# Optimization experiments

Hardware: AMD Instinct MI355X
Metric: run time of the kernel (lower is better)

The kernel has to match this reference:

```python
import jax, jax.numpy as jnp
import numpy as np

B, S, DIN, D, H, DOUT, W = 4, 2048, 256, 512, 8, 128, 64
HD = D // H


def setup_inputs() -> dict:
    key = jax.random.key(0)
    ks = jax.random.split(key, 16)
    r = lambda k, shape, s=0.02: (jax.random.normal(k, shape, jnp.float32) * s)
    return dict(
        x=jax.random.normal(ks[0], (B, S, DIN), jnp.float32),
        pos=jax.random.normal(ks[1], (1, S, D), jnp.float32),  # torch.randn init
        win_w=r(ks[2], (DIN, D)), win_b=jnp.zeros((D,), jnp.float32),
        l_wqkv=r(ks[3], (3, D, D)), l_bqkv=jnp.zeros((3, D), jnp.float32),
        l_wo=r(ks[4], (D, D)), l_bo=jnp.zeros((D,), jnp.float32),
        g_wqkv=r(ks[5], (3, D, D)), g_bqkv=jnp.zeros((3, D), jnp.float32),
        g_wo=r(ks[6], (D, D)), g_bo=jnp.zeros((D,), jnp.float32),
        gate_w=r(ks[7], (2 * D, D)), gate_b=jnp.zeros((D,), jnp.float32),
        ffn_w1=r(ks[8], (D, 2 * D)), ffn_b1=jnp.zeros((2 * D,), jnp.float32),
        ffn_w2=r(ks[9], (2 * D, D)), ffn_b2=jnp.zeros((D,), jnp.float32),
        n1_g=jnp.ones((D,), jnp.float32), n1_b=jnp.zeros((D,), jnp.float32),
        n2_g=jnp.ones((D,), jnp.float32), n2_b=jnp.zeros((D,), jnp.float32),
        n3_g=jnp.ones((D,), jnp.float32), n3_b=jnp.zeros((D,), jnp.float32),
        out_w=r(ks[10], (D, DOUT)), out_b=jnp.zeros((DOUT,), jnp.float32),
    )


def _ln(x, g, b, eps=1e-5):
    m = x.mean(-1, keepdims=True)
    v = ((x - m) ** 2).mean(-1, keepdims=True)
    return (x - m) * jax.lax.rsqrt(v + eps) * g + b


def _mha(x, wqkv, bqkv, wo, bo, mask):
    b, s, d = x.shape
    q = (x @ wqkv[0] + bqkv[0]).reshape(b, s, H, HD)
    k = (x @ wqkv[1] + bqkv[1]).reshape(b, s, H, HD)
    v = (x @ wqkv[2] + bqkv[2]).reshape(b, s, H, HD)
    scores = jnp.einsum('bqhd,bkhd->bhqk', q, k) / np.sqrt(HD).astype(np.float32)
    if mask is not None:
        scores = scores + mask  # additive -inf band mask
    attn = jax.nn.softmax(scores, axis=-1)
    o = jnp.einsum('bhqk,bkhd->bqhd', attn, v).reshape(b, s, d)
    return o @ wo + bo


def reference(x, pos, win_w, win_b,
              l_wqkv, l_bqkv, l_wo, l_bo,
              g_wqkv, g_bqkv, g_wo, g_bo,
              gate_w, gate_b, ffn_w1, ffn_b1, ffn_w2, ffn_b2,
              n1_g, n1_b, n2_g, n2_b, n3_g, n3_b, out_w, out_b):
    s = x.shape[1]
    # band mask: row i allows cols [i - W//2, i + W//2] (matches create_local_mask)
    idx = jnp.arange(s)
    band = jnp.abs(idx[:, None] - idx[None, :]) <= (W // 2)
    mask = jnp.where(band, 0.0, -jnp.inf).astype(jnp.float32)

    h = x @ win_w + win_b + pos
    local_out = _mha(h, l_wqkv, l_bqkv, l_wo, l_bo, mask)
    global_out = _mha(h, g_wqkv, g_bqkv, g_wo, g_bo, None)

    combined = jnp.concatenate([local_out, global_out], axis=-1)
    gate = jnp.tanh(jax.nn.relu(combined @ gate_w + gate_b))
    fused = gate * local_out + (1.0 - gate) * global_out

    h = _ln(h + fused, n1_g, n1_b)
    ffn = jax.nn.relu(h @ ffn_w1 + ffn_b1) @ ffn_w2 + ffn_b2
    h = _ln(h + ffn, n2_g, n2_b)
    h = _ln(h, n3_g, n3_b)
    pooled = h.mean(axis=1)  # AdaptiveAvgPool1d(1) over seq
    return pooled @ out_w + out_b
```

## Files before the change

kernel.cpp:

```cpp
#include <hip/hip_runtime.h>
#include <math.h>
#include <stdint.h>

#define S_LEN 2048
#define DMODEL 512
#define NHEAD 8
#define BATCH 4
#define M_ROWS (BATCH * S_LEN)
#define UAC 4194304

typedef __attribute__((ext_vector_type(8))) short frag8;
typedef __attribute__((ext_vector_type(4))) float f32x4;

__device__ inline unsigned short f2bf(float f) {
    unsigned int u = __float_as_uint(f);
    return (unsigned short)((u + 0x7FFFu + ((u >> 16) & 1u)) >> 16);
}
__device__ inline float bf2f(unsigned short h) {
    return __uint_as_float(((unsigned int)h) << 16);
}

#if __has_builtin(__builtin_amdgcn_exp2f)
#define EXP2(x) __builtin_amdgcn_exp2f(x)
#else
#define EXP2(x) __expf(0.6931471805599453f * (x))
#endif

#if __has_builtin(__builtin_amdgcn_global_load_lds)
__device__ __forceinline__ void glds16(const void* g, void* l, int lane) {
    __builtin_amdgcn_global_load_lds(
        (__attribute__((address_space(1))) void*)(uintptr_t)g,
        (__attribute__((address_space(3))) void*)(uintptr_t)l, 16, 0, 0);
    (void)lane;
}
#else
__device__ __forceinline__ void glds16(const void* g, void* l, int lane) {
    ((uint4*)l)[lane] = ((const uint4*)g)[0];
}
#endif

struct WSeg { const float* src; unsigned short* dst; int K; int N; int start; };
struct WTab { WSeg s[13]; };

__global__ __launch_bounds__(256) void wcast_all(WTab tab)
{
    __shared__ float t[32][33];
    const int bid = blockIdx.x;
    int si = 0;
#pragma unroll
    for (int i = 1; i < 13; ++i) if (bid >= tab.s[i].start) si = i;
    const WSeg sg = tab.s[si];
    const int tile = bid - sg.start;
    if (sg.N == 0) {
        const size_t i = ((size_t)tile * 256 + threadIdx.x) * 8;
        float4 a = *(const float4*)&sg.src[i], b = *(const float4*)&sg.src[i + 4];
        unsigned short us[8];
        us[0] = f2bf(a.x); us[1] = f2bf(a.y); us[2] = f2bf(a.z); us[3] = f2bf(a.w);
        us[4] = f2bf(b.x); us[5] = f2bf(b.y); us[6] = f2bf(b.z); us[7] = f2bf(b.w);
        *(uint4*)&sg.dst[i] = *(uint4*)us;
        return;
    }
    const int nk = sg.K >> 5;
    const int k0 = (tile % nk) * 32, n0 = (tile / nk) * 32;
    {
        int kk = threadIdx.x >> 3, nq = (threadIdx.x & 7) * 4;
        float4 v = *(const float4*)&sg.src[(size_t)(k0 + kk) * sg.N + n0 + nq];
        t[kk][nq + 0] = v.x; t[kk][nq + 1] = v.y; t[kk][nq + 2] = v.z; t[kk][nq + 3] = v.w;
    }
    __syncthreads();
    {
        int n = threadIdx.x >> 3, kq = (threadIdx.x & 7) * 4;
        ushort4 o;
        o.x = f2bf(t[kq + 0][n]); o.y = f2bf(t[kq + 1][n]);
        o.z = f2bf(t[kq + 2][n]); o.w = f2bf(t[kq + 3][n]);
        *(ushort4*)&sg.dst[(size_t)(n0 + n) * sg.K + k0 + kq] = o;
    }
}

__global__ __launch_bounds__(256) void vtrans2_kernel(
    const unsigned short* __restrict__ Vl, const unsigned short* __restrict__ Vg,
    unsigned short* __restrict__ VTl, unsigned short* __restrict__ VTg)
{
    __shared__ unsigned short T[64][72];
    const unsigned short* V = blockIdx.z ? Vg : Vl;
    unsigned short* Vt = blockIdx.z ? VTg : VTl;
    const int st = blockIdx.x, bh = blockIdx.y;
    const int b = bh >> 3, h = bh & 7;
    const int tid = threadIdx.x;
    {
        const int s = tid >> 2, d0 = (tid & 3) * 16;
        const unsigned short* src = V + ((size_t)(b * S_LEN + st * 64 + s) * DMODEL + h * 64 + d0);
        *(uint4*)&T[s][d0] = *(const uint4*)src;
        *(uint4*)&T[s][d0 + 8] = *(const uint4*)(src + 8);
    }
    __syncthreads();
    {
        const int d = tid >> 2, s0 = (tid & 3) * 16;
        unsigned short buf[16];
#pragma unroll
        for (int j = 0; j < 16; ++j) buf[j] = T[s0 + j][d];
        unsigned short* dst = Vt + ((size_t)(bh * 64 + d) * S_LEN + st * 64 + s0);
        *(uint4*)&dst[0] = *(const uint4*)&buf[0];
        *(uint4*)&dst[8] = *(const uint4*)&buf[8];
    }
}

template <int MODE, int BN>
__global__ __launch_bounds__(256) void gemm_mfma(
    const unsigned short* __restrict__ A, const unsigned short* __restrict__ A2,
    const unsigned short* __restrict__ Wt, const float* __restrict__ bias,
    const float* __restrict__ bias2, const float* __restrict__ pos,
    unsigned short* __restrict__ C, unsigned short* __restrict__ C2,
    int M, int N, int K)
{
    constexpr int UN = BN / 32;
    __shared__ unsigned short As[128 * 64];
    __shared__ unsigned short Bs[BN * 64];
    const int tid = threadIdx.x;
    const int wave = tid >> 6, lane = tid & 63;
    const int lr = lane & 15, quad = lane >> 4;
    const int bm = blockIdx.x * 128, bn = blockIdx.y * BN;
    const int rm = (wave >> 1) * 64, rn = (wave & 1) * (BN / 2);
    const int Khalf = K >> 1;
    const int KA = (MODE == 3) ? Khalf : K;

    const unsigned short* SA = A;
    const unsigned short* SW = Wt;
    const float* SBIAS = bias;
    unsigned short* SC = C;
    if constexpr (MODE == 6) {
        if (blockIdx.z) { SA = A2; SW = Wt + 512 * 512; SBIAS = bias2; SC = C2; }
    }

    const int lrow = lane >> 3;
    const int gch = ((lane & 7) - lrow) & 7;
    const size_t laneA = (size_t)(bm + wave * 32 + lrow) * KA + gch * 8;
    const size_t laneB = (size_t)(bn + wave * (BN / 4) + lrow) * K + gch * 8;
    unsigned short* ldsA = As + wave * 2048;
    unsigned short* ldsB = Bs + wave * (BN * 16);

    f32x4 acc[4][UN];
#pragma unroll
    for (int t = 0; t < 4; ++t)
#pragma unroll
        for (int u = 0; u < UN; ++u) acc[t][u] = (f32x4){0.f, 0.f, 0.f, 0.f};

    const int sw0 = ((quad + lr) & 7) * 8;
    const int sw1 = ((quad + lr + 4) & 7) * 8;

    for (int k0 = 0; k0 < K; k0 += 64) {
        __syncthreads();
        const unsigned short* Ab; int kadj;
        if constexpr (MODE == 3) { Ab = (k0 < Khalf) ? A : A2; kadj = k0 & (Khalf - 1); }
        else { Ab = SA; kadj = k0; }
        const unsigned short* pa = Ab + laneA + kadj;
        glds16(pa,           ldsA,        lane);
        glds16(pa + 8 * KA,  ldsA + 512,  lane);
        glds16(pa + 16 * KA, ldsA + 1024, lane);
        glds16(pa + 24 * KA, ldsA + 1536, lane);
        const unsigned short* pb = SW + laneB + k0;
#pragma unroll
        for (int i = 0; i < UN; ++i)
            glds16(pb + i * 8 * K, ldsB + i * 512, lane);
        __syncthreads();

#pragma unroll
        for (int kc = 0; kc < 2; ++kc) {
            const int sw = kc ? sw1 : sw0;
            frag8 af[4], bf[UN];
#pragma unroll
            for (int t = 0; t < 4; ++t)
                af[t] = *(const frag8*)&As[(rm + t * 16 + lr) * 64 + sw];
#pragma unroll
            for (int u = 0; u < UN; ++u)
                bf[u] = *(const frag8*)&Bs[(rn + u * 16 + lr) * 64 + sw];
#pragma unroll
            for (int t = 0; t < 4; ++t)
#pragma unroll
                for (int u = 0; u < UN; ++u)
                    acc[t][u] = __builtin_amdgcn_mfma_f32_16x16x32_bf16(
                        af[t], bf[u], acc[t][u], 0, 0, 0);
        }
    }

#pragma unroll
    for (int t = 0; t < 4; ++t) {
#pragma unroll
        for (int i = 0; i < 4; ++i) {
            const int m = bm + rm + t * 16 + quad * 4 + i;
#pragma unroll
            for (int u = 0; u < UN; ++u) {
                const int n = bn + rn + u * 16 + lr;
                if constexpr (MODE == 5) {
                    const int mat = n >> 9;
                    const int nn = n & 511;
                    const float* bp = (mat < 3) ? (bias + (mat << 9))
                                                : (bias2 + ((mat - 3) << 9));
                    float v = acc[t][u][i] + bp[nn];
                    if (mat == 0 || mat == 3) v *= 0.18033688011112042f;
                    C[(size_t)mat * UAC + (size_t)m * DMODEL + nn] = f2bf(v);
                } else {
                    float v = acc[t][u][i] + SBIAS[n];
                    if constexpr (MODE == 1) v += pos[(size_t)(m & (S_LEN - 1)) * N + n];
                    if constexpr (MODE == 2) v = fmaxf(v, 0.0f);
                    if constexpr (MODE == 3) {
                        float g = tanhf(fmaxf(v, 0.0f));
                        float lo = bf2f(A[(size_t)m * Khalf + n]);
                        float go = bf2f(A2[(size_t)m * Khalf + n]);
                        v = g * lo + (1.0f - g) * go;
                    }
                    SC[(size_t)m * N + n] = f2bf(v);
                }
            }
        }
    }
}

__global__ __launch_bounds__(256) void attn_mfma(
    const unsigned short* __restrict__ Ql, const unsigned short* __restrict__ Kl,
    const unsigned short* __restrict__ VTl, unsigned short* __restrict__ AOl,
    const unsigned short* __restrict__ Qg, const unsigned short* __restrict__ Kg,
    const unsigned short* __restrict__ VTg, unsigned short* __restrict__ AOg)
{
    __shared__ unsigned short Ks[64 * 64];
    __shared__ unsigned short Vts[64 * 64];
    __shared__ unsigned short Ps[64 * 64];
    const int qt = blockIdx.x, h = blockIdx.y;
    const int glob = blockIdx.z < 4;
    const int b = blockIdx.z & 3;
    const int masked = !glob;
    const unsigned short* Q  = glob ? Qg  : Ql;
    const unsigned short* Kv = glob ? Kg  : Kl;
    const unsigned short* Vt = glob ? VTg : VTl;
    unsigned short* O        = glob ? AOg : AOl;
    const int tid = threadIdx.x;
    const int wave = tid >> 6, lane = tid & 63;
    const int lr = lane & 15, quad = lane >> 4;

    {
        const int q = tid >> 2, c8 = (tid & 3) * 2;
        const unsigned short* src = Q + ((size_t)(b * S_LEN + qt * 64 + q) * DMODEL + h * 64 + c8 * 8);
        *(uint4*)&Ps[q * 64 + (((c8 + q) & 7) * 8)] = *(const uint4*)src;
        *(uint4*)&Ps[q * 64 + (((c8 + 1 + q) & 7) * 8)] = *(const uint4*)(src + 8);
    }
    const int sw0 = ((quad + lr) & 7) * 8;
    const int sw1 = ((quad + lr + 4) & 7) * 8;
    const int prow = (wave * 16 + lr) * 64;
    frag8 qf[2];
    qf[0] = *(const frag8*)&Ps[prow + sw0];
    qf[1] = *(const frag8*)&Ps[prow + sw1];

    f32x4 oacc[4];
#pragma unroll
    for (int t = 0; t < 4; ++t) oacc[t] = (f32x4){0.f, 0.f, 0.f, 0.f};
    float l_r = 0.f;

    int kt0 = 0, kt1 = 31;
    if (masked) { kt0 = qt > 0 ? qt - 1 : 0; kt1 = qt < 31 ? qt + 1 : 31; }

    const int lrow = lane >> 3;
    const int gch = ((lane & 7) - lrow) & 7;
    const unsigned short* kp = Kv + ((size_t)(b * S_LEN + kt0 * 64 + wave * 16 + lrow) * DMODEL + h * 64 + gch * 8);
    const unsigned short* vp = Vt + ((size_t)((b * 8 + h) * 64 + wave * 16 + lrow) * S_LEN + kt0 * 64 + gch * 8);
    unsigned short* lk = Ks + wave * 1024;
    unsigned short* lv = Vts + wave * 1024;

    for (int kt = kt0; kt <= kt1; ++kt) {
        __syncthreads();
        glds16(kp, lk, lane);
        glds16(kp + 8 * DMODEL, lk + 512, lane);
        glds16(vp, lv, lane);
        glds16(vp + 8 * S_LEN, lv + 512, lane);
        kp += 64 * DMODEL; vp += 64;
        __syncthreads();

        f32x4 sacc[4];
#pragma unroll
        for (int t = 0; t < 4; ++t) sacc[t] = (f32x4){0.f, 0.f, 0.f, 0.f};
#pragma unroll
        for (int kc = 0; kc < 2; ++kc) {
            const int sw = kc ? sw1 : sw0;
#pragma unroll
            for (int t = 0; t < 4; ++t) {
                frag8 kf = *(const frag8*)&Ks[(t * 16 + lr) * 64 + sw];
                sacc[t] = __builtin_amdgcn_mfma_f32_16x16x32_bf16(kf, qf[kc], sacc[t], 0, 0, 0);
            }
        }

#pragma unroll
        for (int t = 0; t < 4; ++t) {
            float p0 = EXP2(sacc[t][0]);
            float p1 = EXP2(sacc[t][1]);
            float p2 = EXP2(sacc[t][2]);
            float p3 = EXP2(sacc[t][3]);
            if (masked) {
                const int qa = qt * 64 + wave * 16 + lr;
                const int ca = kt * 64 + t * 16 + quad * 4;
                int d0 = qa - ca;
                if (d0 > 32 || d0 < -32) p0 = 0.f;
                int d1 = qa - (ca + 1);
                if (d1 > 32 || d1 < -32) p1 = 0.f;
                int d2 = qa - (ca + 2);
                if (d2 > 32 || d2 < -32) p2 = 0.f;
                int d3 = qa - (ca + 3);
                if (d3 > 32 || d3 < -32) p3 = 0.f;
            }
            const unsigned u0 = __float_as_uint(p0) & 0xFFFF0000u;
            const unsigned u1 = __float_as_uint(p1) & 0xFFFF0000u;
            const unsigned u2 = __float_as_uint(p2) & 0xFFFF0000u;
            const unsigned u3 = __float_as_uint(p3) & 0xFFFF0000u;
            l_r += (__uint_as_float(u0) + __uint_as_float(u1)) +
                   (__uint_as_float(u2) + __uint_as_float(u3));
            uint2 pw;
            pw.x = __builtin_amdgcn_perm(u1, u0, 0x07060302);
            pw.y = __builtin_amdgcn_perm(u3, u2, 0x07060302);
            const int slot = ((2 * t + (quad >> 1) + lr) & 7) * 8 + (quad & 1) * 4;
            *(uint2*)&Ps[prow + slot] = pw;
        }

#pragma unroll
        for (int cc = 0; cc < 2; ++cc) {
            const int sw = cc ? sw1 : sw0;
            frag8 pa = *(const frag8*)&Ps[prow + sw];
#pragma unroll
            for (int t = 0; t < 4; ++t) {
                frag8 vf = *(const frag8*)&Vts[(t * 16 + lr) * 64 + sw];
                oacc[t] = __builtin_amdgcn_mfma_f32_16x16x32_bf16(pa, vf, oacc[t], 0, 0, 0);
            }
        }
    }

    l_r += __shfl_xor(l_r, 16);
    l_r += __shfl_xor(l_r, 32);
#pragma unroll
    for (int i = 0; i < 4; ++i) {
        const float inv = 1.0f / __shfl(l_r, quad * 4 + i);
        const int q = qt * 64 + wave * 16 + quad * 4 + i;
#pragma unroll
        for (int t = 0; t < 4; ++t)
            O[(size_t)(b * S_LEN + q) * DMODEL + h * 64 + t * 16 + lr] = f2bf(oacc[t][i] * inv);
    }
}

__device__ inline float wave_sum64(float v) {
#pragma unroll
    for (int off = 1; off < 64; off <<= 1) v += __shfl_xor(v, off);
    return v;
}

__global__ __launch_bounds__(256) void ln_res_kernel(
    const unsigned short* __restrict__ A, const unsigned short* __restrict__ Bb,
    const float* __restrict__ g, const float* __restrict__ be,
    unsigned short* __restrict__ out)
{
    const size_t row = blockIdx.x * 4 + (threadIdx.x >> 6);
    const int lane = threadIdx.x & 63;
    float x[8]; float s = 0.f;
#pragma unroll
    for (int k = 0; k < 8; ++k) {
        size_t idx = row * DMODEL + k * 64 + lane;
        x[k] = bf2f(A[idx]) + bf2f(Bb[idx]);
        s += x[k];
    }
    s = wave_sum64(s);
    float mean = s * (1.0f / DMODEL);
    float v = 0.f;
#pragma unroll
    for (int k = 0; k < 8; ++k) { float d = x[k] - mean; v += d * d; }
    v = wave_sum64(v) * (1.0f / DMODEL);
    float r = rsqrtf(v + 1e-5f);
#pragma unroll
    for (int k = 0; k < 8; ++k)
        out[row * DMODEL + k * 64 + lane] =
            f2bf((x[k] - mean) * r * g[k * 64 + lane] + be[k * 64 + lane]);
}

__global__ __launch_bounds__(256) void ln_double_kernel(
    const unsigned short* __restrict__ A, const unsigned short* __restrict__ Bb,
    const float* __restrict__ g2, const float* __restrict__ b2,
    const float* __restrict__ g3, const float* __restrict__ b3,
    unsigned short* __restrict__ out)
{
    const size_t row = blockIdx.x * 4 + (threadIdx.x >> 6);
    const int lane = threadIdx.x & 63;
    float x[8]; float s = 0.f;
#pragma unroll
    for (int k = 0; k < 8; ++k) {
        size_t idx = row * DMODEL + k * 64 + lane;
        x[k] = bf2f(A[idx]) + bf2f(Bb[idx]);
        s += x[k];
    }
    s = wave_sum64(s);
    float mean = s * (1.0f / DMODEL);
    float v = 0.f;
#pragma unroll
    for (int k = 0; k < 8; ++k) { float d = x[k] - mean; v += d * d; }
    v = wave_sum64(v) * (1.0f / DMODEL);
    float r = rsqrtf(v + 1e-5f);
    float t[8]; float s2 = 0.f;
#pragma unroll
    for (int k = 0; k < 8; ++k) {
        t[k] = (x[k] - mean) * r * g2[k * 64 + lane] + b2[k * 64 + lane];
        s2 += t[k];
    }
    s2 = wave_sum64(s2);
    float mean2 = s2 * (1.0f / DMODEL);
    float v2 = 0.f;
#pragma unroll
    for (int k = 0; k < 8; ++k) { float d = t[k] - mean2; v2 += d * d; }
    v2 = wave_sum64(v2) * (1.0f / DMODEL);
    float r2 = rsqrtf(v2 + 1e-5f);
#pragma unroll
    for (int k = 0; k < 8; ++k)
        out[row * DMODEL + k * 64 + lane] =
            f2bf((t[k] - mean2) * r2 * g3[k * 64 + lane] + b3[k * 64 + lane]);
}

__global__ __launch_bounds__(256) void pool_kernel(
    const unsigned short* __restrict__ h2, float* __restrict__ partials)
{
    const int b = blockIdx.x >> 4;
    const int chunk = blockIdx.x & 15;
    const int tid = threadIdx.x;
    float s0 = 0.f, s1 = 0.f;
    size_t base = (size_t)(b * S_LEN + chunk * 128) * DMODEL;
    for (int r = 0; r < 128; ++r) {
        s0 += bf2f(h2[base + (size_t)r * DMODEL + tid]);
        s1 += bf2f(h2[base + (size_t)r * DMODEL + 256 + tid]);
    }
    partials[(size_t)(b * 16 + chunk) * DMODEL + tid] = s0;
    partials[(size_t)(b * 16 + chunk) * DMODEL + 256 + tid] = s1;
}

__global__ __launch_bounds__(128) void out_kernel(
    const float* __restrict__ partials, const float* __restrict__ w,
    const float* __restrict__ bias, float* __restrict__ out)
{
    __shared__ float pooled[DMODEL];
    const int b = blockIdx.x;
    const int o = threadIdx.x;
#pragma unroll
    for (int j = 0; j < 4; ++j) {
        const int d = j * 128 + o;
        float s = 0.f;
#pragma unroll
        for (int c = 0; c < 16; ++c)
            s += partials[(size_t)(b * 16 + c) * DMODEL + d];
        pooled[d] = s;
    }
    __syncthreads();
    float acc = 0.f;
    for (int d = 0; d < DMODEL; ++d)
        acc += pooled[d] * w[d * 128 + o];
    out[b * 128 + o] = acc * (1.0f / S_LEN) + bias[o];
}

extern "C" void kernel_launch(void* const* d_in, const int* in_sizes, int n_in,
                              void* d_out, int out_size, void* d_ws, size_t ws_size,
                              hipStream_t stream)
{
    const float* x      = (const float*)d_in[0];
    const float* pos    = (const float*)d_in[1];
    const float* win_w  = (const float*)d_in[2];
    const float* win_b  = (const float*)d_in[3];
    const float* l_wqkv = (const float*)d_in[4];
    const float* l_bqkv = (const float*)d_in[5];
    const float* l_wo   = (const float*)d_in[6];
    const float* l_bo   = (const float*)d_in[7];
    const float* g_wqkv = (const float*)d_in[8];
    const float* g_bqkv = (const float*)d_in[9];
    const float* g_wo   = (const float*)d_in[10];
    const float* g_bo   = (const float*)d_in[11];
    const float* gate_w = (const float*)d_in[12];
    const float* gate_b = (const float*)d_in[13];
    const float* ffn_w1 = (const float*)d_in[14];
    const float* ffn_b1 = (const float*)d_in[15];
    const float* ffn_w2 = (const float*)d_in[16];
    const float* ffn_b2 = (const float*)d_in[17];
    const float* n1_g   = (const float*)d_in[18];
    const float* n1_b   = (const float*)d_in[19];
    const float* n2_g   = (const float*)d_in[20];
    const float* n2_b   = (const float*)d_in[21];
    const float* n3_g   = (const float*)d_in[22];
    const float* n3_b   = (const float*)d_in[23];
    const float* out_w  = (const float*)d_in[24];
    const float* out_b  = (const float*)d_in[25];
    float* out = (float*)d_out;

    unsigned short* ws16 = (unsigned short*)d_ws;
    const size_t UA = (size_t)UAC;
    unsigned short* H    = ws16 + 0 * UA;
    unsigned short* QKV  = ws16 + 1 * UA;
    unsigned short* Ql   = ws16 + 1 * UA;
    unsigned short* Kl   = ws16 + 2 * UA;
    unsigned short* Vl   = ws16 + 3 * UA;
    unsigned short* Qg   = ws16 + 4 * UA;
    unsigned short* Kg   = ws16 + 5 * UA;
    unsigned short* Vg   = ws16 + 6 * UA;
    unsigned short* VTl  = ws16 + 7 * UA;
    unsigned short* AOl    = Vl;
    unsigned short* LO     = Kl;
    unsigned short* GO     = Qg;
    unsigned short* FUSED  = Kg;
    unsigned short* H1     = Vg;
    unsigned short* FFNMID = Vl;
    unsigned short* FFNOUT = Ql;
    unsigned short* H2     = Kl;

    unsigned short* wt = ws16 + 8 * UA;
    unsigned short* win_t  = wt;
    unsigned short* lqkv_t = win_t  + 131072;
    unsigned short* gqkv_t = lqkv_t + 786432;
    unsigned short* lwo_t  = gqkv_t + 786432;
    unsigned short* gwo_t  = lwo_t  + 262144;
    unsigned short* gate_t = gwo_t  + 262144;
    unsigned short* ffn1_t = gate_t + 524288;
    unsigned short* ffn2_t = ffn1_t + 524288;
    unsigned short* xb     = ffn2_t + 524288;
    unsigned short* VTg    = xb + 2097152;
    unsigned short* AOg    = VTg + UA;
    float* PARTIALS = (float*)(void*)(AOg + UA);

    WTab tab;
    tab.s[0]  = {win_w,             win_t,             256,  512,    0};
    tab.s[1]  = {l_wqkv + 0*262144, lqkv_t + 0*262144, 512,  512,  128};
    tab.s[2]  = {l_wqkv + 1*262144, lqkv_t + 1*262144, 512,  512,  384};
    tab.s[3]  = {l_wqkv + 2*262144, lqkv_t + 2*262144, 512,  512,  640};
    tab.s[4]  = {g_wqkv + 0*262144, gqkv_t + 0*262144, 512,  512,  896};
    tab.s[5]  = {g_wqkv + 1*262144, gqkv_t + 1*262144, 512,  512, 1152};
    tab.s[6]  = {g_wqkv + 2*262144, gqkv_t + 2*262144, 512,  512, 1408};
    tab.s[7]  = {l_wo,              lwo_t,             512,  512, 1664};
    tab.s[8]  = {g_wo,              gwo_t,             512,  512, 1920};
    tab.s[9]  = {gate_w,            gate_t,            1024, 512, 2176};
    tab.s[10] = {ffn_w1,            ffn1_t,            512, 1024, 2688};
    tab.s[11] = {ffn_w2,            ffn2_t,            1024, 512, 3200};
    tab.s[12] = {x,                 xb,                0,    0,   3712};

    dim3 blk(256);
    wcast_all<<<dim3(4736), blk, 0, stream>>>(tab);

    dim3 gD(M_ROWS / 128, 512 / 64);
    dim3 gW(M_ROWS / 128, 512 / 64, 2);
    dim3 gQ(M_ROWS / 128, 3072 / 128);
    dim3 gF(M_ROWS / 128, 1024 / 128);
    dim3 gAT(S_LEN / 64, NHEAD, 2*BATCH);
    dim3 gV(S_LEN / 64, BATCH * NHEAD, 2);

    gemm_mfma<1, 64><<<gD, blk, 0, stream>>>(xb, nullptr, win_t, win_b, nullptr, pos, H, nullptr, M_ROWS, 512, 256);

    gemm_mfma<5, 128><<<gQ, blk, 0, stream>>>(H, nullptr, lqkv_t, l_bqkv, g_bqkv, nullptr, QKV, nullptr, M_ROWS, 3072, 512);

    vtrans2_kernel<<<gV, blk, 0, stream>>>(Vl, Vg, VTl, VTg);

    attn_mfma<<<gAT, blk, 0, stream>>>(Ql, Kl, VTl, AOl, Qg, Kg, VTg, AOg);

    gemm_mfma<6, 64><<<gW, blk, 0, stream>>>(AOl, AOg, lwo_t, l_bo, g_bo, nullptr, LO, GO, M_ROWS, 512, 512);

    gemm_mfma<3, 64><<<gD, blk, 0, stream>>>(LO, GO, gate_t, gate_b, nullptr, nullptr, FUSED, nullptr, M_ROWS, 512, 1024);

    ln_res_kernel<<<M_ROWS / 4, blk, 0, stream>>>(H, FUSED, n1_g, n1_b, H1);

    gemm_mfma<2, 128><<<gF, blk, 0, stream>>>(H1, nullptr, ffn1_t, ffn_b1, nullptr, nullptr, FFNMID, nullptr, M_ROWS, 1024, 512);
    gemm_mfma<0, 64><<<gD, blk, 0, stream>>>(FFNMID, nullptr, ffn2_t, ffn_b2, nullptr, nullptr, FFNOUT, nullptr, M_ROWS, 512, 1024);

    ln_double_kernel<<<M_ROWS / 4, blk, 0, stream>>>(H1, FFNOUT, n2_g, n2_b, n3_g, n3_b, H2);

    pool_kernel<<<dim3(BATCH * 16), blk, 0, stream>>>(H2, PARTIALS);
    out_kernel<<<dim3(BATCH), dim3(128), 0, stream>>>(PARTIALS, out_w, out_b, out);
}
```

Measured before the change: 345.2 us.

## Fuse layernorms into GEMM epilogues via last-block atomic counters, merge pool and output

Removes the standalone layernorm kernels. The last of the 8 column-tile blocks for each 128-row stripe, found with an atomic counter, reruns layernorm over that stripe inside the gate GEMM and the FFN2 GEMM. The pool and output kernels are merged the same way, with the last pool block computing the final projection. Counters are zeroed in the weight-cast kernel. This saves launches and one global round trip per layernorm, but the LN work is serialized onto a few tail blocks, one per row stripe, which may lengthen the GEMM tail.

```diff
diff --git a/kernel.cpp b/kernel.cpp
--- a/kernel.cpp
+++ b/kernel.cpp
@@ -39,13 +39,20 @@
 }
 #endif
 
+__device__ inline float wave_sum64(float v) {
+#pragma unroll
+    for (int off = 1; off < 64; off <<= 1) v += __shfl_xor(v, off);
+    return v;
+}
+
 struct WSeg { const float* src; unsigned short* dst; int K; int N; int start; };
-struct WTab { WSeg s[13]; };
+struct WTab { WSeg s[13]; int* cnt; };
 
 __global__ __launch_bounds__(256) void wcast_all(WTab tab)
 {
     __shared__ float t[32][33];
     const int bid = blockIdx.x;
+    if (bid == 0 && threadIdx.x < 129) tab.cnt[threadIdx.x] = 0;
     int si = 0;
 #pragma unroll
     for (int i = 1; i < 13; ++i) if (bid >= tab.s[i].start) si = i;
@@ -105,13 +112,21 @@
     }
 }
 
+struct LNArgs {
+    const float* g1; const float* b1;
+    const float* g2; const float* b2;
+    const unsigned short* resid;
+    unsigned short* lnout;
+    int* cnt;
+};
+
 template <int MODE, int BN>
 __global__ __launch_bounds__(256) void gemm_mfma(
     const unsigned short* __restrict__ A, const unsigned short* __restrict__ A2,
     const unsigned short* __restrict__ Wt, const float* __restrict__ bias,
     const float* __restrict__ bias2, const float* __restrict__ pos,
     unsigned short* __restrict__ C, unsigned short* __restrict__ C2,
-    int M, int N, int K)
+    int M, int N, int K, LNArgs ln)
 {
     constexpr int UN = BN / 32;
     __shared__ unsigned short As[128 * 64];
@@ -211,6 +226,58 @@
                     }
                     SC[(size_t)m * N + n] = f2bf(v);
                 }
+            }
+        }
+    }
+
+    if constexpr (MODE == 3 || MODE == 7) {
+        __shared__ int lastflag;
+        __threadfence();
+        __syncthreads();
+        if (tid == 0) lastflag = atomicAdd(ln.cnt + blockIdx.x, 1);
+        __syncthreads();
+        if (lastflag != 7) return;
+        __threadfence();
+        const int lane2 = tid & 63, w2 = tid >> 6;
+        for (int p = 0; p < 32; ++p) {
+            const size_t row = (size_t)blockIdx.x * 128 + p * 4 + w2;
+            float xv[8]; float s = 0.f;
+#pragma unroll
+            for (int k = 0; k < 8; ++k) {
+                const size_t idx = row * DMODEL + k * 64 + lane2;
+                xv[k] = bf2f(ln.resid[idx]) + bf2f(SC[idx]);
+                s += xv[k];
+            }
+            s = wave_sum64(s);
+            float mean = s * (1.0f / DMODEL);
+            float var = 0.f;
+#pragma unroll
+            for (int k = 0; k < 8; ++k) { float d = xv[k] - mean; var += d * d; }
+            var = wave_sum64(var) * (1.0f / DMODEL);
+            float r = rsqrtf(var + 1e-5f);
+            if constexpr (MODE == 3) {
+#pragma unroll
+                for (int k = 0; k < 8; ++k)
+                    ln.lnout[row * DMODEL + k * 64 + lane2] =
+                        f2bf((xv[k] - mean) * r * ln.g1[k * 64 + lane2] + ln.b1[k * 64 + lane2]);
+            } else {
+                float tv[8]; float s2 = 0.f;
+#pragma unroll
+                for (int k = 0; k < 8; ++k) {
+                    tv[k] = (xv[k] - mean) * r * ln.g1[k * 64 + lane2] + ln.b1[k * 64 + lane2];
+                    s2 += tv[k];
+                }
+                s2 = wave_sum64(s2);
+                float mean2 = s2 * (1.0f / DMODEL);
+                float v2 = 0.f;
+#pragma unroll
+                for (int k = 0; k < 8; ++k) { float d = tv[k] - mean2; v2 += d * d; }
+                v2 = wave_sum64(v2) * (1.0f / DMODEL);
+                float r2 = rsqrtf(v2 + 1e-5f);
+#pragma unroll
+                for (int k = 0; k < 8; ++k)
+                    ln.lnout[row * DMODEL + k * 64 + lane2] =
+                        f2bf((tv[k] - mean2) * r2 * ln.g2[k * 64 + lane2] + ln.b2[k * 64 + lane2]);
             }
         }
     }
@@ -342,83 +409,13 @@
     }
 }
 
-__device__ inline float wave_sum64(float v) {
-#pragma unroll
-    for (int off = 1; off < 64; off <<= 1) v += __shfl_xor(v, off);
-    return v;
-}
-
-__global__ __launch_bounds__(256) void ln_res_kernel(
-    const unsigned short* __restrict__ A, const unsigned short* __restrict__ Bb,
-    const float* __restrict__ g, const float* __restrict__ be,
-    unsigned short* __restrict__ out)
+__global__ __launch_bounds__(256) void pool_kernel(
+    const unsigned short* __restrict__ h2, float* __restrict__ partials,
+    const float* __restrict__ w, const float* __restrict__ bias,
+    float* __restrict__ out, int* __restrict__ cnt)
 {
-    const size_t row = blockIdx.x * 4 + (threadIdx.x >> 6);
-    const int lane = threadIdx.x & 63;
-    float x[8]; float s = 0.f;
-#pragma unroll
-    for (int k = 0; k < 8; ++k) {
-        size_t idx = row * DMODEL + k * 64 + lane;
-        x[k] = bf2f(A[idx]) + bf2f(Bb[idx]);
-        s += x[k];
-    }
-    s = wave_sum64(s);
-    float mean = s * (1.0f / DMODEL);
-    float v = 0.f;
-#pragma unroll
-    for (int k = 0; k < 8; ++k) { float d = x[k] - mean; v += d * d; }
-    v = wave_sum64(v) * (1.0f / DMODEL);
-    float r = rsqrtf(v + 1e-5f);
-#pragma unroll
-    for (int k = 0; k < 8; ++k)
-        out[row * DMODEL + k * 64 + lane] =
-            f2bf((x[k] - mean) * r * g[k * 64 + lane] + be[k * 64 + lane]);
-}
-
-__global__ __launch_bounds__(256) void ln_double_kernel(
-    const unsigned short* __restrict__ A, const unsigned short* __restrict__ Bb,
-    const float* __restrict__ g2, const float* __restrict__ b2,
-    const float* __restrict__ g3, const float* __restrict__ b3,
-    unsigned short* __restrict__ out)
-{
-    const size_t row = blockIdx.x * 4 + (threadIdx.x >> 6);
-    const int lane = threadIdx.x & 63;
-    float x[8]; float s = 0.f;
-#pragma unroll
-    for (int k = 0; k < 8; ++k) {
-        size_t idx = row * DMODEL + k * 64 + lane;
-        x[k] = bf2f(A[idx]) + bf2f(Bb[idx]);
-        s += x[k];
-    }
-    s = wave_sum64(s);
-    float mean = s * (1.0f / DMODEL);
-    float v = 0.f;
-#pragma unroll
-    for (int k = 0; k < 8; ++k) { float d = x[k] - mean; v += d * d; }
-    v = wave_sum64(v) * (1.0f / DMODEL);
-    float r = rsqrtf(v + 1e-5f);
-    float t[8]; float s2 = 0.f;
-#pragma unroll
-    for (int k = 0; k < 8; ++k) {
-        t[k] = (x[k] - mean) * r * g2[k * 64 + lane] + b2[k * 64 + lane];
-        s2 += t[k];
-    }
-    s2 = wave_sum64(s2);
-    float mean2 = s2 * (1.0f / DMODEL);
-    float v2 = 0.f;
-#pragma unroll
-    for (int k = 0; k < 8; ++k) { float d = t[k] - mean2; v2 += d * d; }
-    v2 = wave_sum64(v2) * (1.0f / DMODEL);
-    float r2 = rsqrtf(v2 + 1e-5f);
-#pragma unroll
-    for (int k = 0; k < 8; ++k)
-        out[row * DMODEL + k * 64 + lane] =
-            f2bf((t[k] - mean2) * r2 * g3[k * 64 + lane] + b3[k * 64 + lane]);
-}
-
-__global__ __launch_bounds__(256) void pool_kernel(
-    const unsigned short* __restrict__ h2, float* __restrict__ partials)
-{
+    __shared__ float pooled[DMODEL];
+    __shared__ int lastflag;
     const int b = blockIdx.x >> 4;
     const int chunk = blockIdx.x & 15;
     const int tid = threadIdx.x;
@@ -430,29 +427,33 @@
     }
     partials[(size_t)(b * 16 + chunk) * DMODEL + tid] = s0;
     partials[(size_t)(b * 16 + chunk) * DMODEL + 256 + tid] = s1;
-}
-
-__global__ __launch_bounds__(128) void out_kernel(
-    const float* __restrict__ partials, const float* __restrict__ w,
-    const float* __restrict__ bias, float* __restrict__ out)
-{
-    __shared__ float pooled[DMODEL];
-    const int b = blockIdx.x;
-    const int o = threadIdx.x;
-#pragma unroll
-    for (int j = 0; j < 4; ++j) {
-        const int d = j * 128 + o;
-        float s = 0.f;
-#pragma unroll
-        for (int c = 0; c < 16; ++c)
-            s += partials[(size_t)(b * 16 + c) * DMODEL + d];
-        pooled[d] = s;
-    }
+
+    __threadfence();
     __syncthreads();
-    float acc = 0.f;
-    for (int d = 0; d < DMODEL; ++d)
-        acc += pooled[d] * w[d * 128 + o];
-    out[b * 128 + o] = acc * (1.0f / S_LEN) + bias[o];
+    if (tid == 0) lastflag = atomicAdd(cnt, 1);
+    __syncthreads();
+    if (lastflag != 63) return;
+    __threadfence();
+
+    for (int bb = 0; bb < BATCH; ++bb) {
+#pragma unroll
+        for (int j = 0; j < 2; ++j) {
+            const int d = j * 256 + tid;
+            float s = 0.f;
+#pragma unroll
+            for (int c = 0; c < 16; ++c)
+                s += partials[(size_t)(bb * 16 + c) * DMODEL + d];
+            pooled[d] = s;
+        }
+        __syncthreads();
+        if (tid < 128) {
+            float acc = 0.f;
+            for (int d = 0; d < DMODEL; ++d)
+                acc += pooled[d] * w[d * 128 + tid];
+            out[bb * 128 + tid] = acc * (1.0f / S_LEN) + bias[tid];
+        }
+        __syncthreads();
+    }
 }
 
 extern "C" void kernel_launch(void* const* d_in, const int* in_sizes, int n_in,
@@ -520,6 +521,7 @@
     unsigned short* VTg    = xb + 2097152;
     unsigned short* AOg    = VTg + UA;
     float* PARTIALS = (float*)(void*)(AOg + UA);
+    int*   CNT      = (int*)(PARTIALS + 64 * 512);
 
     WTab tab;
     tab.s[0]  = {win_w,             win_t,             256,  512,    0};
@@ -535,6 +537,11 @@
     tab.s[10] = {ffn_w1,            ffn1_t,            512, 1024, 2688};
     tab.s[11] = {ffn_w2,            ffn2_t,            1024, 512, 3200};
     tab.s[12] = {x,                 xb,                0,    0,   3712};
+    tab.cnt = CNT;
+
+    const LNArgs noln = {nullptr, nullptr, nullptr, nullptr, nullptr, nullptr, nullptr};
+    const LNArgs ln1  = {n1_g, n1_b, nullptr, nullptr, H,  H1, CNT};
+    const LNArgs ln2  = {n2_g, n2_b, n3_g, n3_b,       H1, H2, CNT + 64};
 
     dim3 blk(256);
     wcast_all<<<dim3(4736), blk, 0, stream>>>(tab);
@@ -546,25 +553,21 @@
     dim3 gAT(S_LEN / 64, NHEAD, 2*BATCH);
     dim3 gV(S_LEN / 64, BATCH * NHEAD, 2);
 
-    gemm_mfma<1, 64><<<gD, blk, 0, stream>>>(xb, nullptr, win_t, win_b, nullptr, pos, H, nullptr, M_ROWS, 512, 256);
-
-    gemm_mfma<5, 128><<<gQ, blk, 0, stream>>>(H, nullptr, lqkv_t, l_bqkv, g_bqkv, nullptr, QKV, nullptr, M_ROWS, 3072, 512);
+    gemm_mfma<1, 64><<<gD, blk, 0, stream>>>(xb, nullptr, win_t, win_b, nullptr, pos, H, nullptr, M_ROWS, 512, 256, noln);
+
+    gemm_mfma<5, 128><<<gQ, blk, 0, stream>>>(H, nullptr, lqkv_t, l_bqkv, g_bqkv, nullptr, QKV, nullptr, M_ROWS, 3072, 512, noln);
 
     vtrans2_kernel<<<gV, blk, 0, stream>>>(Vl, Vg, VTl, VTg);
 
     attn_mfma<<<gAT, blk, 0, stream>>>(Ql, Kl, VTl, AOl, Qg, Kg, VTg, AOg);
 
-    gemm_mfma<6, 64><<<gW, blk, 0, stream>>>(AOl, AOg, lwo_t, l_bo, g_bo, nullptr, LO, GO, M_ROWS, 512, 512);
-
-    gemm_mfma<3, 64><<<gD, blk, 0, stream>>>(LO, GO, gate_t, gate_b, nullptr, nullptr, FUSED, nullptr, M_ROWS, 512, 1024);
-
-    ln_res_kernel<<<M_ROWS / 4, blk, 0, stream>>>(H, FUSED, n1_g, n1_b, H1);
-
-    gemm_mfma<2, 128><<<gF, blk, 0, stream>>>(H1, nullptr, ffn1_t, ffn_b1, nullptr, nullptr, FFNMID, nullptr, M_ROWS, 1024, 512);
-    gemm_mfma<0, 64><<<gD, blk, 0, stream>>>(FFNMID, nullptr, ffn2_t, ffn_b2, nullptr, nullptr, FFNOUT, nullptr, M_ROWS, 512, 1024);
-
-    ln_double_kernel<<<M_ROWS / 4, blk, 0, stream>>>(H1, FFNOUT, n2_g, n2_b, n3_g, n3_b, H2);
-
-    pool_kernel<<<dim3(BATCH * 16), blk, 0, stream>>>(H2, PARTIALS);
-    out_kernel<<<dim3(BATCH), dim3(128), 0, stream>>>(PARTIALS, out_w, out_b, out);
-}
+    gemm_mfma<6, 64><<<gW, blk, 0, stream>>>(AOl, AOg, lwo_t, l_bo, g_bo, nullptr, LO, GO, M_ROWS, 512, 512, noln);
+
+    gemm_mfma<3, 64><<<gD, blk, 0, stream>>>(LO, GO, gate_t, gate_b, nullptr, nullptr, FUSED, nullptr, M_ROWS, 512, 1024, ln1);
+
+    gemm_mfma<2, 128><<<gF, blk, 0, stream>>>(H1, nullptr, ffn1_t, ffn_b1, nullptr, nullptr, FFNMID, nullptr, M_ROWS, 1024, 512, noln);
+
+    gemm_mfma<7, 64><<<gD, blk, 0, stream>>>(FFNMID, nullptr, ffn2_t, ffn_b2, nullptr, nullptr, FFNOUT, nullptr, M_ROWS, 512, 1024, ln2);
+
+    pool_kernel<<<dim3(BATCH * 16), blk, 0, stream>>>(H2, PARTIALS, out_w, out_b, out, CNT + 128);
+}
```

After: 551.3 us. 1.6x slower.
